# Kernel tuning notes

Measured on AMD Instinct MI355X. Metric: run time of the kernel, lower is better.

Reference implementation:

```python
import jax, jax.numpy as jnp
import numpy as np

B, H, W, C = 16, 64, 64, 512
HEADS, WS, SHIFT = 16, 8, 4
N = WS * WS            # tokens per window
HID = 4 * C            # mlp hidden


def _buffers():
    # Swin-V2 log-spaced continuous relative coords table [1, 2ws-1, 2ws-1, 2]
    rc = np.arange(-(WS - 1), WS, dtype=np.float32)
    table = np.stack(np.meshgrid(rc, rc, indexing='ij'), axis=-1)[None]
    table = table / (WS - 1) * 8.0
    table = np.sign(table) * np.log2(np.abs(table) + 1.0) / np.log2(8.0)
    # relative position index [N, N]
    coords = np.stack(np.meshgrid(np.arange(WS), np.arange(WS), indexing='ij')).reshape(2, -1)
    rel = (coords[:, :, None] - coords[:, None, :]).transpose(1, 2, 0)
    rel[..., 0] += WS - 1
    rel[..., 1] += WS - 1
    rel[..., 0] *= 2 * WS - 1
    idx = rel.sum(-1).astype(np.int32)
    # shifted-window attention mask [nW, N, N]
    img = np.zeros((H, W), dtype=np.float32)
    sl = (slice(0, -WS), slice(-WS, -SHIFT), slice(-SHIFT, None))
    cnt = 0
    for hs in sl:
        for ws_ in sl:
            img[hs, ws_] = cnt
            cnt += 1
    mw = img.reshape(H // WS, WS, W // WS, WS).transpose(0, 2, 1, 3).reshape(-1, N)
    am = mw[:, None, :] - mw[:, :, None]
    am = np.where(am != 0, np.float32(-100.0), np.float32(0.0)).astype(np.float32)
    return table.astype(np.float32), idx, am


def setup_inputs() -> dict:
    key = jax.random.key(0)
    ks = jax.random.split(key, 8)
    table, idx, am = _buffers()
    p = lambda k, s: jax.random.normal(k, s, jnp.float32) * 0.02
    return {
        'x': jax.random.normal(ks[0], (B, H * W, C), jnp.float32),
        'qkv_w': p(ks[1], (3 * C, C)),
        'q_bias': jnp.zeros((C,), jnp.float32),
        'v_bias': jnp.zeros((C,), jnp.float32),
        'logit_scale': jnp.full((HEADS, 1, 1), np.log(10.0), jnp.float32),
        'cpb_w1': p(ks[2], (512, 2)),
        'cpb_b1': jnp.zeros((512,), jnp.float32),
        'cpb_w2': p(ks[3], (HEADS, 512)),
        'proj_w': p(ks[4], (C, C)),
        'proj_b': jnp.zeros((C,), jnp.float32),
        'norm1_g': jnp.ones((C,), jnp.float32),
        'norm1_b': jnp.zeros((C,), jnp.float32),
        'norm2_g': jnp.ones((C,), jnp.float32),
        'norm2_b': jnp.zeros((C,), jnp.float32),
        'fc1_w': p(ks[5], (HID, C)),
        'fc1_b': jnp.zeros((HID,), jnp.float32),
        'fc2_w': p(ks[6], (C, HID)),
        'fc2_b': jnp.zeros((C,), jnp.float32),
        'coords_table': jnp.asarray(table),
        'attn_mask': jnp.asarray(am),
        'rel_pos_index': jnp.asarray(idx),
    }


def _layernorm(x, g, b):
    m = x.mean(-1, keepdims=True)
    v = ((x - m) ** 2).mean(-1, keepdims=True)
    return (x - m) / jnp.sqrt(v + 1e-5) * g + b


def reference(x, qkv_w, q_bias, v_bias, logit_scale, cpb_w1, cpb_b1, cpb_w2,
              proj_w, proj_b, norm1_g, norm1_b, norm2_g, norm2_b,
              fc1_w, fc1_b, fc2_w, fc2_b, coords_table, attn_mask, rel_pos_index):
    Bsz, L, Cd = x.shape
    d = Cd // HEADS
    shortcut = x
    # cyclic shift + window partition: [B*nW, N, C]
    xr = jnp.roll(x.reshape(Bsz, H, W, Cd), (-SHIFT, -SHIFT), axis=(1, 2))
    xw = xr.reshape(Bsz, H // WS, WS, W // WS, WS, Cd).transpose(0, 1, 3, 2, 4, 5).reshape(-1, N, Cd)
    B_ = xw.shape[0]
    nW = B_ // Bsz
    # qkv with q/v-only bias
    qkv_bias = jnp.concatenate([q_bias, jnp.zeros_like(v_bias), v_bias])
    qkv = (xw @ qkv_w.T + qkv_bias).reshape(B_, N, 3, HEADS, d).transpose(2, 0, 3, 1, 4)
    q, k, v = qkv[0], qkv[1], qkv[2]  # [B_, h, N, d]
    # cosine attention with learned clamped logit scale
    qn = q / jnp.maximum(jnp.linalg.norm(q, axis=-1, keepdims=True), 1e-12)
    kn = k / jnp.maximum(jnp.linalg.norm(k, axis=-1, keepdims=True), 1e-12)
    scale = jnp.exp(jnp.minimum(logit_scale, jnp.log(jnp.float32(100.0))))
    attn = jnp.einsum('bhnd,bhmd->bhnm', qn, kn) * scale
    # CPB MLP relative position bias
    tbl = jax.nn.relu(coords_table @ cpb_w1.T + cpb_b1) @ cpb_w2.T  # [1,2ws-1,2ws-1,h]
    rpb = tbl.reshape(-1, HEADS)[rel_pos_index.reshape(-1)].reshape(N, N, HEADS).transpose(2, 0, 1)
    attn = attn + 16.0 * jax.nn.sigmoid(rpb)[None]
    # shift mask
    attn = (attn.reshape(Bsz, nW, HEADS, N, N) + attn_mask[None, :, None]).reshape(B_, HEADS, N, N)
    attn = jax.nn.softmax(attn, axis=-1)
    out = jnp.einsum('bhnm,bhmd->bhnd', attn, v).transpose(0, 2, 1, 3).reshape(B_, N, Cd)
    out = out @ proj_w.T + proj_b
    # window reverse + reverse shift
    out = out.reshape(Bsz, H // WS, W // WS, WS, WS, Cd).transpose(0, 1, 3, 2, 4, 5).reshape(Bsz, H, W, Cd)
    out = jnp.roll(out, (SHIFT, SHIFT), axis=(1, 2)).reshape(Bsz, L, Cd)
    # Swin-V2 post-norm residuals
    x1 = shortcut + _layernorm(out, norm1_g, norm1_b)
    mlp = jax.nn.gelu(x1 @ fc1_w.T + fc1_b, approximate=False) @ fc2_w.T + fc2_b
    return x1 + _layernorm(mlp, norm2_g, norm2_b)
```

## Files before the change

### kernel.cpp

```cpp
#include <hip/hip_runtime.h>
#include <hip/hip_bf16.h>
#include <math.h>

#define BB     16
#define HH     64
#define WWID   64
#define CCH    512
#define HEADS  16
#define NTOK   64
#define DDIM   32
#define NWIN   64
#define LL     (HH*WWID)
#define MTOT   (BB*LL)
#define BWIN   (BB*NWIN)
#define HIDN   2048
#define SHIFT_ 4

typedef unsigned short u16;
using bf16x8 = __attribute__((ext_vector_type(8))) short;
using f32x4  = __attribute__((ext_vector_type(4))) float;
using f32x16 = __attribute__((ext_vector_type(16))) float;

__device__ __forceinline__ u16 f2bf(float f) {
  union { float f; unsigned u; } v; v.f = f;
  unsigned r = v.u + 0x7fffu + ((v.u >> 16) & 1u);
  return (u16)(r >> 16);
}
__device__ __forceinline__ float bf2f(unsigned h) {
  union { unsigned u; float f; } v; v.u = h << 16;
  return v.f;
}

__device__ __forceinline__ void gload16(const void* g, void* l) {
  __builtin_amdgcn_global_load_lds((const __attribute__((address_space(1))) void*)g,
                                   (__attribute__((address_space(3))) void*)l, 16, 0, 0);
}

__device__ __forceinline__ int win2orig(int b_, int n) {
  int b = b_ >> 6, wi = b_ & 63;
  int hs = (wi >> 3) * 8 + (n >> 3);
  int ws = (wi & 7) * 8 + (n & 7);
  int hq = (hs + SHIFT_) & 63;
  int wq = (ws + SHIFT_) & 63;
  return b * LL + hq * WWID + wq;
}

__global__ void cvt_k(const float* __restrict__ s, u16* __restrict__ d, int n) {
  int i = blockIdx.x * 256 + threadIdx.x;
  if (i < n) d[i] = f2bf(s[i]);
}

__global__ void cpb_k(const float* __restrict__ ct, const float* __restrict__ w1,
                      const float* __restrict__ b1, const float* __restrict__ w2,
                      float* __restrict__ t2) {
  int t = blockIdx.x * 256 + threadIdx.x;
  if (t >= 225 * 16) return;
  int rr = t >> 4, h = t & 15;
  float c0 = ct[rr * 2], c1 = ct[rr * 2 + 1];
  float acc = 0.f;
  for (int j = 0; j < 512; j++) {
    float hv = fmaxf(w1[j * 2] * c0 + w1[j * 2 + 1] * c1 + b1[j], 0.f);
    acc += hv * w2[h * 512 + j];
  }
  t2[t] = acc;
}

__global__ void bias_k(const float* __restrict__ t2, const int* __restrict__ rpi,
                       float* __restrict__ b16) {
  int t = blockIdx.x * 256 + threadIdx.x;
  int nm = t & 4095;
  int h = t >> 12;
  float v = t2[rpi[nm] * 16 + h];
  b16[t] = 16.0f / (1.0f + __expf(-v));
}

__global__ void scale_k(const float* __restrict__ ls, float* __restrict__ sc) {
  int t = threadIdx.x;
  if (t < HEADS) sc[t] = __expf(fminf(ls[t], 4.6051701859880914f));
}

__global__ __launch_bounds__(256) void xw_k(const float* __restrict__ x, u16* __restrict__ xw) {
  int t = blockIdx.x * 256 + threadIdx.x;
  int row = t >> 6;
  int col = (t & 63) * 8;
  const float* src = x + (size_t)win2orig(row >> 6, row & 63) * CCH + col;
  float4 a = *(const float4*)src;
  float4 b = *(const float4*)(src + 4);
  u16 o[8] = {f2bf(a.x), f2bf(a.y), f2bf(a.z), f2bf(a.w),
              f2bf(b.x), f2bf(b.y), f2bf(b.z), f2bf(b.w)};
  *(uint4*)(xw + (size_t)row * CCH + col) = *(const uint4*)o;
}

template<int MODE, int NBN>
__global__ __launch_bounds__(256, 2) void gemm256_k(
    const u16* __restrict__ A, const u16* __restrict__ Bw,
    const float* __restrict__ bias,
    const float* __restrict__ qbias, const float* __restrict__ vbias,
    u16* __restrict__ o0, u16* __restrict__ o1, u16* __restrict__ o2,
    int K, int mchunk)
{
  __shared__ __align__(16) u16 smem[3 * 12288];
  const int t = threadIdx.x;
  const int lin = blockIdx.x;
  const int xcd = lin & 7;
  const int j = lin >> 3;
  const int m0 = (xcd * mchunk + j / NBN) * 256;
  const int n0 = (j % NBN) * 128;
  const int lane = t & 63;
  const int wv = t >> 6;
  const int wm = (wv & 1) * 128;
  const int wn = (wv >> 1) * 64;
  const int l31 = lane & 31;
  const int khalf = lane >> 5;
  const int sw = lane & 3;

  const int swcol = (((t & 3) ^ ((t >> 2) & 3)) * 8);
  const u16* aP[4]; int aL[4];
  #pragma unroll
  for (int i = 0; i < 4; i++) {
    aP[i] = A + (size_t)(m0 + i * 64 + (t >> 2)) * K + swcol;
    aL[i] = i * 4096 + wv * 1024;
  }
  const u16* bP[2]; int bL[2];
  #pragma unroll
  for (int i = 0; i < 2; i++) {
    bP[i] = Bw + (size_t)(n0 + i * 64 + (t >> 2)) * K + swcol;
    bL[i] = 16384 + i * 4096 + wv * 1024;
  }

  f32x16 acc[4][2] = {};

  auto stage = [&](int k0, int bi) {
    char* base = (char*)smem + bi * 24576;
    #pragma unroll
    for (int i = 0; i < 4; i++) gload16(aP[i] + k0, base + aL[i]);
    #pragma unroll
    for (int i = 0; i < 2; i++) gload16(bP[i] + k0, base + bL[i]);
  };

  const int NT = K >> 5;
  stage(0, 0);
  stage(32, 1);

  for (int it = 0; it < NT; ++it) {
    if (it + 1 < NT) asm volatile("s_waitcnt vmcnt(6)" ::: "memory");
    else             asm volatile("s_waitcnt vmcnt(0)" ::: "memory");
    __builtin_amdgcn_s_barrier();
    asm volatile("" ::: "memory");
    if (it + 2 < NT) stage((it + 2) << 5, (it + 2) % 3);

    const u16* Ab = (const u16*)((const char*)smem + (it % 3) * 24576);
    const u16* Bb = Ab + 8192;
    #pragma unroll
    for (int ks = 0; ks < 2; ks++) {
      const int kc = (ks * 2 + khalf) ^ sw;
      bf16x8 af[4], bf[2];
      #pragma unroll
      for (int mt = 0; mt < 4; mt++)
        af[mt] = *(const bf16x8*)&Ab[(wm + mt * 32 + l31) * 32 + kc * 8];
      #pragma unroll
      for (int nt = 0; nt < 2; nt++)
        bf[nt] = *(const bf16x8*)&Bb[(wn + nt * 32 + l31) * 32 + kc * 8];
      #pragma unroll
      for (int mt = 0; mt < 4; mt++)
        #pragma unroll
        for (int nt = 0; nt < 2; nt++)
          acc[mt][nt] = __builtin_amdgcn_mfma_f32_32x32x16_bf16(bf[nt], af[mt], acc[mt][nt], 0, 0, 0);
    }
  }

  const int part = n0 >> 9;
  u16* qkvdst = (MODE == 0) ? (part == 0 ? o0 : (part == 1 ? o1 : o2)) : o0;
  #pragma unroll
  for (int mt = 0; mt < 4; mt++) {
    const int grow = m0 + wm + mt * 32 + l31;
    size_t rowbase;
    if (MODE == 0) {
      int b_ = grow >> 6, n = grow & 63;
      rowbase = ((size_t)b_ * HEADS) * (NTOK * DDIM) + (size_t)n * DDIM;
    } else if (MODE == 1) {
      rowbase = (size_t)win2orig(grow >> 6, grow & 63) * CCH;
    } else if (MODE == 2) {
      rowbase = (size_t)grow * HIDN;
    } else {
      rowbase = (size_t)grow * CCH;
    }
    #pragma unroll
    for (int nt = 0; nt < 2; nt++) {
      const int cb = n0 + wn + nt * 32;
      unsigned U[4], W[4];
      #pragma unroll
      for (int g = 0; g < 4; g++) {
        const int nb = cb + 8 * g + 4 * khalf;
        float v0 = acc[mt][nt][g * 4 + 0];
        float v1 = acc[mt][nt][g * 4 + 1];
        float v2 = acc[mt][nt][g * 4 + 2];
        float v3 = acc[mt][nt][g * 4 + 3];
        if (MODE == 0) {
          const int cc = nb & 511;
          if (part == 0) {
            float4 b4 = *(const float4*)(qbias + cc);
            v0 += b4.x; v1 += b4.y; v2 += b4.z; v3 += b4.w;
          } else if (part == 2) {
            float4 b4 = *(const float4*)(vbias + cc);
            v0 += b4.x; v1 += b4.y; v2 += b4.z; v3 += b4.w;
          }
        } else {
          float4 b4 = *(const float4*)(bias + nb);
          v0 += b4.x; v1 += b4.y; v2 += b4.z; v3 += b4.w;
          if (MODE == 2) {
            v0 = 0.5f * v0 * (1.0f + erff(v0 * 0.70710678118654752f));
            v1 = 0.5f * v1 * (1.0f + erff(v1 * 0.70710678118654752f));
            v2 = 0.5f * v2 * (1.0f + erff(v2 * 0.70710678118654752f));
            v3 = 0.5f * v3 * (1.0f + erff(v3 * 0.70710678118654752f));
          }
        }
        U[g] = (unsigned)f2bf(v0) | ((unsigned)f2bf(v1) << 16);
        W[g] = (unsigned)f2bf(v2) | ((unsigned)f2bf(v3) << 16);
      }
      asm volatile("v_permlane32_swap_b32 %0, %1" : "+v"(U[0]), "+v"(U[1]));
      asm volatile("v_permlane32_swap_b32 %0, %1" : "+v"(W[0]), "+v"(W[1]));
      asm volatile("v_permlane32_swap_b32 %0, %1" : "+v"(U[2]), "+v"(U[3]));
      asm volatile("v_permlane32_swap_b32 %0, %1" : "+v"(W[2]), "+v"(W[3]));
      uint4 s1 = make_uint4(U[0], W[0], U[1], W[1]);
      uint4 s2 = make_uint4(U[2], W[2], U[3], W[3]);
      if (MODE == 0) {
        const int cc1 = (cb & 511) + 8 * khalf;
        const int cc2 = cc1 + 16;
        *(uint4*)(qkvdst + rowbase + (size_t)(cc1 >> 5) * (NTOK * DDIM) + (cc1 & 31)) = s1;
        *(uint4*)(qkvdst + rowbase + (size_t)(cc2 >> 5) * (NTOK * DDIM) + (cc2 & 31)) = s2;
      } else {
        *(uint4*)(o0 + rowbase + cb + 8 * khalf) = s1;
        *(uint4*)(o0 + rowbase + cb + 16 + 8 * khalf) = s2;
      }
    }
  }
}

__global__ __launch_bounds__(64) void attn_k(
    const u16* __restrict__ qb, const u16* __restrict__ kb, const u16* __restrict__ vb,
    const float* __restrict__ bias16, const float* __restrict__ scale,
    const float* __restrict__ amask, u16* __restrict__ attn_out)
{
  __shared__ u16 Pmat[64][72];
  __shared__ u16 vT[32][72];

  int bh = blockIdx.x;
  int b_ = bh >> 4, h = bh & 15;
  int wi = b_ & 63;
  int lane = threadIdx.x;
  int l15 = lane & 15, quad = lane >> 4;
  const u16* qs = qb + (size_t)bh * (NTOK * DDIM);
  const u16* ks = kb + (size_t)bh * (NTOK * DDIM);
  const u16* vs = vb + (size_t)bh * (NTOK * DDIM);

  bf16x8 qf[4], kf[4];
  #pragma unroll
  for (int mt = 0; mt < 4; mt++) {
    qf[mt] = *(const bf16x8*)(qs + (mt * 16 + l15) * DDIM + quad * 8);
    kf[mt] = *(const bf16x8*)(ks + (mt * 16 + l15) * DDIM + quad * 8);
  }
  #pragma unroll
  for (int mt = 0; mt < 4; mt++) {
    float sq = 0.f, sk = 0.f;
    #pragma unroll
    for (int jj = 0; jj < 8; jj++) {
      float a = bf2f((u16)qf[mt][jj]); sq += a * a;
      float b = bf2f((u16)kf[mt][jj]); sk += b * b;
    }
    sq += __shfl_xor(sq, 16); sq += __shfl_xor(sq, 32);
    sk += __shfl_xor(sk, 16); sk += __shfl_xor(sk, 32);
    float iq = 1.f / fmaxf(sqrtf(sq), 1e-12f);
    float ik = 1.f / fmaxf(sqrtf(sk), 1e-12f);
    #pragma unroll
    for (int jj = 0; jj < 8; jj++) {
      qf[mt][jj] = (short)f2bf(bf2f((u16)qf[mt][jj]) * iq);
      kf[mt][jj] = (short)f2bf(bf2f((u16)kf[mt][jj]) * ik);
    }
  }
  f32x4 s[4][4];
  #pragma unroll
  for (int mt = 0; mt < 4; mt++)
    #pragma unroll
    for (int nt = 0; nt < 4; nt++) {
      f32x4 c = {0.f, 0.f, 0.f, 0.f};
      s[mt][nt] = __builtin_amdgcn_mfma_f32_16x16x32_bf16(qf[mt], kf[nt], c, 0, 0, 0);
    }
  #pragma unroll
  for (int d8 = 0; d8 < 4; d8++) {
    bf16x8 vv = *(const bf16x8*)(vs + lane * DDIM + d8 * 8);
    #pragma unroll
    for (int jj = 0; jj < 8; jj++) vT[d8 * 8 + jj][lane] = (u16)vv[jj];
  }

  float sc = scale[h];
  float rinv[4][4];
  const float* bbase = bias16 + (size_t)h * 4096;
  const float* mbase = amask + (size_t)wi * 4096;
  #pragma unroll
  for (int mt = 0; mt < 4; mt++) {
    #pragma unroll
    for (int i = 0; i < 4; i++) {
      int row = mt * 16 + quad * 4 + i;
      const float* bro = bbase + row * 64;
      const float* mro = mbase + row * 64;
      float p[4];
      float mx = -1e30f;
      #pragma unroll
      for (int nt = 0; nt < 4; nt++) {
        int col = nt * 16 + l15;
        float vv = s[mt][nt][i] * sc + bro[col] + mro[col];
        p[nt] = vv;
        mx = fmaxf(mx, vv);
      }
      mx = fmaxf(mx, __shfl_xor(mx, 1));
      mx = fmaxf(mx, __shfl_xor(mx, 2));
      mx = fmaxf(mx, __shfl_xor(mx, 4));
      mx = fmaxf(mx, __shfl_xor(mx, 8));
      float sum = 0.f;
      #pragma unroll
      for (int nt = 0; nt < 4; nt++) {
        float e = __expf(p[nt] - mx);
        p[nt] = e;
        sum += e;
      }
      sum += __shfl_xor(sum, 1);
      sum += __shfl_xor(sum, 2);
      sum += __shfl_xor(sum, 4);
      sum += __shfl_xor(sum, 8);
      rinv[mt][i] = 1.f / sum;
      #pragma unroll
      for (int nt = 0; nt < 4; nt++)
        Pmat[row][nt * 16 + l15] = f2bf(p[nt]);
    }
  }
  __syncthreads();

  f32x4 oacc[4][2] = {};
  #pragma unroll
  for (int ks2 = 0; ks2 < 2; ks2++) {
    bf16x8 pf[4], vf[2];
    #pragma unroll
    for (int mt = 0; mt < 4; mt++)
      pf[mt] = *(const bf16x8*)&Pmat[mt * 16 + l15][ks2 * 32 + quad * 8];
    #pragma unroll
    for (int nt = 0; nt < 2; nt++)
      vf[nt] = *(const bf16x8*)&vT[nt * 16 + l15][ks2 * 32 + quad * 8];
    #pragma unroll
    for (int mt = 0; mt < 4; mt++)
      #pragma unroll
      for (int nt = 0; nt < 2; nt++)
        oacc[mt][nt] = __builtin_amdgcn_mfma_f32_16x16x32_bf16(pf[mt], vf[nt], oacc[mt][nt], 0, 0, 0);
  }
  #pragma unroll
  for (int mt = 0; mt < 4; mt++)
    #pragma unroll
    for (int nt = 0; nt < 2; nt++)
      #pragma unroll
      for (int i = 0; i < 4; i++) {
        int n = mt * 16 + quad * 4 + i;
        int d = nt * 16 + l15;
        float val = oacc[mt][nt][i] * rinv[mt][i];
        attn_out[(size_t)(b_ * 64 + n) * CCH + h * DDIM + d] = f2bf(val);
      }
}

__global__ __launch_bounds__(256) void ln_res_k(
    const float* __restrict__ xin, const u16* __restrict__ pin,
    const float* __restrict__ gam, const float* __restrict__ bet,
    float* __restrict__ x1f, u16* __restrict__ x1b)
{
  int row = blockIdx.x * 4 + (threadIdx.x >> 6);
  int lane = threadIdx.x & 63;
  size_t base = (size_t)row * CCH + lane * 8;
  uint4 u = *(const uint4*)(pin + base);
  unsigned w[4] = {u.x, u.y, u.z, u.w};
  float pv[8];
  #pragma unroll
  for (int j = 0; j < 4; j++) {
    pv[j * 2] = bf2f(w[j] & 0xffffu);
    pv[j * 2 + 1] = bf2f(w[j] >> 16);
  }
  const float* xr = xin + base;
  float s = 0.f, sq = 0.f;
  #pragma unroll
  for (int j = 0; j < 8; j++) { s += pv[j]; sq += pv[j] * pv[j]; }
  #pragma unroll
  for (int o = 32; o > 0; o >>= 1) { s += __shfl_xor(s, o, 64); sq += __shfl_xor(sq, o, 64); }
  float mean = s * (1.0f / 512.0f);
  float var = sq * (1.0f / 512.0f) - mean * mean;
  float rstd = rsqrtf(var + 1e-5f);
  #pragma unroll
  for (int j = 0; j < 8; j++) {
    int c = lane * 8 + j;
    float val = xr[j] + (pv[j] - mean) * rstd * gam[c] + bet[c];
    x1f[base + j] = val;
    x1b[base + j] = f2bf(val);
  }
}

__global__ __launch_bounds__(256) void ln_fin_k(
    const u16* __restrict__ mlp, const float* __restrict__ gam,
    const float* __restrict__ bet, float* __restrict__ io)
{
  int row = blockIdx.x * 4 + (threadIdx.x >> 6);
  int lane = threadIdx.x & 63;
  size_t base = (size_t)row * CCH + lane * 8;
  uint4 u = *(const uint4*)(mlp + base);
  unsigned w[4] = {u.x, u.y, u.z, u.w};
  float pv[8];
  #pragma unroll
  for (int j = 0; j < 4; j++) {
    pv[j * 2] = bf2f(w[j] & 0xffffu);
    pv[j * 2 + 1] = bf2f(w[j] >> 16);
  }
  float s = 0.f, sq = 0.f;
  #pragma unroll
  for (int j = 0; j < 8; j++) { s += pv[j]; sq += pv[j] * pv[j]; }
  #pragma unroll
  for (int o = 32; o > 0; o >>= 1) { s += __shfl_xor(s, o, 64); sq += __shfl_xor(sq, o, 64); }
  float mean = s * (1.0f / 512.0f);
  float var = sq * (1.0f / 512.0f) - mean * mean;
  float rstd = rsqrtf(var + 1e-5f);
  #pragma unroll
  for (int j = 0; j < 8; j++) {
    int c = lane * 8 + j;
    io[base + j] = io[base + j] + (pv[j] - mean) * rstd * gam[c] + bet[c];
  }
}

#define OFF_Q     ((size_t)0)
#define OFF_K     ((size_t)67108864)
#define OFF_V     ((size_t)134217728)
#define OFF_ATTN  ((size_t)201326592)
#define OFF_X1B   ((size_t)268435456)
#define OFF_WQKV  ((size_t)335544320)
#define OFF_WPROJ ((size_t)337117184)
#define OFF_WFC1  ((size_t)337641472)
#define OFF_WFC2  ((size_t)339738624)
#define OFF_T2    ((size_t)341835776)
#define OFF_B16   ((size_t)341852160)
#define OFF_SC    ((size_t)342114304)

extern "C" void kernel_launch(void* const* d_in, const int* in_sizes, int n_in,
                              void* d_out, int out_size, void* d_ws, size_t ws_size,
                              hipStream_t stream) {
  const float* x        = (const float*)d_in[0];
  const float* qkv_w    = (const float*)d_in[1];
  const float* q_bias   = (const float*)d_in[2];
  const float* v_bias   = (const float*)d_in[3];
  const float* lscale   = (const float*)d_in[4];
  const float* cpb_w1   = (const float*)d_in[5];
  const float* cpb_b1   = (const float*)d_in[6];
  const float* cpb_w2   = (const float*)d_in[7];
  const float* proj_w   = (const float*)d_in[8];
  const float* proj_b   = (const float*)d_in[9];
  const float* n1g      = (const float*)d_in[10];
  const float* n1b      = (const float*)d_in[11];
  const float* n2g      = (const float*)d_in[12];
  const float* n2b      = (const float*)d_in[13];
  const float* fc1_w    = (const float*)d_in[14];
  const float* fc1_b    = (const float*)d_in[15];
  const float* fc2_w    = (const float*)d_in[16];
  const float* fc2_b    = (const float*)d_in[17];
  const float* ctab     = (const float*)d_in[18];
  const float* amask    = (const float*)d_in[19];
  const int*   rpi      = (const int*)d_in[20];

  char* ws = (char*)d_ws;
  float* outp = (float*)d_out;

  u16*   q_buf    = (u16*)(ws + OFF_Q);
  u16*   k_buf    = (u16*)(ws + OFF_K);
  u16*   v_buf    = (u16*)(ws + OFF_V);
  u16*   proj_out = (u16*)(ws + OFF_Q);
  u16*   hid      = (u16*)(ws + OFF_Q);
  u16*   xw       = (u16*)(ws + OFF_ATTN);
  u16*   attn_out = (u16*)(ws + OFF_ATTN);
  u16*   mlp_out  = (u16*)(ws + OFF_ATTN);
  u16*   x1b      = (u16*)(ws + OFF_X1B);
  u16*   wqkv     = (u16*)(ws + OFF_WQKV);
  u16*   wproj    = (u16*)(ws + OFF_WPROJ);
  u16*   wfc1     = (u16*)(ws + OFF_WFC1);
  u16*   wfc2     = (u16*)(ws + OFF_WFC2);
  float* t2       = (float*)(ws + OFF_T2);
  float* b16      = (float*)(ws + OFF_B16);
  float* scbuf    = (float*)(ws + OFF_SC);

  cvt_k<<<(1536 * 512 + 255) / 256, 256, 0, stream>>>(qkv_w, wqkv, 1536 * 512);
  cvt_k<<<(512 * 512 + 255) / 256, 256, 0, stream>>>(proj_w, wproj, 512 * 512);
  cvt_k<<<(2048 * 512 + 255) / 256, 256, 0, stream>>>(fc1_w, wfc1, 2048 * 512);
  cvt_k<<<(512 * 2048 + 255) / 256, 256, 0, stream>>>(fc2_w, wfc2, 512 * 2048);
  cpb_k<<<15, 256, 0, stream>>>(ctab, cpb_w1, cpb_b1, cpb_w2, t2);
  bias_k<<<256, 256, 0, stream>>>(t2, rpi, b16);
  scale_k<<<1, 64, 0, stream>>>(lscale, scbuf);

  xw_k<<<MTOT * 64 / 256, 256, 0, stream>>>(x, xw);
  gemm256_k<0, 12><<<256 * 12, 256, 0, stream>>>(
      xw, wqkv, nullptr, q_bias, v_bias, q_buf, k_buf, v_buf, 512, 32);
  attn_k<<<BWIN * HEADS, 64, 0, stream>>>(q_buf, k_buf, v_buf, b16, scbuf, amask, attn_out);
  gemm256_k<1, 4><<<256 * 4, 256, 0, stream>>>(
      attn_out, wproj, proj_b, nullptr, nullptr, proj_out, nullptr, nullptr, 512, 32);
  ln_res_k<<<MTOT / 4, 256, 0, stream>>>(x, proj_out, n1g, n1b, outp, x1b);
  for (int half = 0; half < 2; half++) {
    const u16* a1 = x1b + (size_t)half * (MTOT / 2) * CCH;
    u16* m1 = mlp_out + (size_t)half * (MTOT / 2) * CCH;
    gemm256_k<2, 16><<<128 * 16, 256, 0, stream>>>(
        a1, wfc1, fc1_b, nullptr, nullptr, hid, nullptr, nullptr, 512, 16);
    gemm256_k<3, 4><<<128 * 4, 256, 0, stream>>>(
        hid, wfc2, fc2_b, nullptr, nullptr, m1, nullptr, nullptr, 2048, 16);
  }
  ln_fin_k<<<MTOT / 4, 256, 0, stream>>>(mlp_out, n2g, n2b, outp);
}
```

Measured before the change: 1.150 ms.

## Use packed bf16 converts, tanh-GELU, new LDS swizzle, vectorized layernorm I/O

Swaps the software bf16 rounding for the hardware v_cvt_pk_bf16_f32 instruction in several kernels. Replaces the exact erf GELU in the fc1 epilogue with a tanh-style sigmoid approximation. Changes the LDS swizzle pattern in the GEMM staging and fragment reads to reduce bank conflicts. Vectorizes the global loads and stores in both layernorm-residual kernels. The GELU approximation changes numerics slightly relative to the exact erf reference.

```diff
diff --git a/kernel.cpp b/kernel.cpp
--- a/kernel.cpp
+++ b/kernel.cpp
@@ -30,6 +30,16 @@
   union { unsigned u; float f; } v; v.u = h << 16;
   return v.f;
 }
+__device__ __forceinline__ unsigned cvtpk(float lo, float hi) {
+  unsigned r;
+  asm("v_cvt_pk_bf16_f32 %0, %1, %2" : "=v"(r) : "v"(lo), "v"(hi));
+  return r;
+}
+__device__ __forceinline__ float gelu_f(float v) {
+  float v3 = v * v * v;
+  float y = 1.5957691216057308f * v + 0.0713548162726009f * v3;
+  return v / (1.f + __expf(-y));
+}
 
 __device__ __forceinline__ void gload16(const void* g, void* l) {
   __builtin_amdgcn_global_load_lds((const __attribute__((address_space(1))) void*)g,
@@ -86,9 +96,9 @@
   const float* src = x + (size_t)win2orig(row >> 6, row & 63) * CCH + col;
   float4 a = *(const float4*)src;
   float4 b = *(const float4*)(src + 4);
-  u16 o[8] = {f2bf(a.x), f2bf(a.y), f2bf(a.z), f2bf(a.w),
-              f2bf(b.x), f2bf(b.y), f2bf(b.z), f2bf(b.w)};
-  *(uint4*)(xw + (size_t)row * CCH + col) = *(const uint4*)o;
+  uint4 o = make_uint4(cvtpk(a.x, a.y), cvtpk(a.z, a.w),
+                       cvtpk(b.x, b.y), cvtpk(b.z, b.w));
+  *(uint4*)(xw + (size_t)row * CCH + col) = o;
 }
 
 template<int MODE, int NBN>
@@ -112,9 +122,9 @@
   const int wn = (wv >> 1) * 64;
   const int l31 = lane & 31;
   const int khalf = lane >> 5;
-  const int sw = lane & 3;
-
-  const int swcol = (((t & 3) ^ ((t >> 2) & 3)) * 8);
+
+  const int sstg = (((t >> 2) + (t >> 4)) & 3);
+  const int swcol = (((t & 3) ^ sstg) * 8);
   const u16* aP[4]; int aL[4];
   #pragma unroll
   for (int i = 0; i < 4; i++) {
@@ -141,6 +151,8 @@
   const int NT = K >> 5;
   stage(0, 0);
   stage(32, 1);
+
+  const int srd = ((l31 & 3) + ((l31 >> 2) & 3)) & 3;
 
   for (int it = 0; it < NT; ++it) {
     if (it + 1 < NT) asm volatile("s_waitcnt vmcnt(6)" ::: "memory");
@@ -153,7 +165,7 @@
     const u16* Bb = Ab + 8192;
     #pragma unroll
     for (int ks = 0; ks < 2; ks++) {
-      const int kc = (ks * 2 + khalf) ^ sw;
+      const int kc = (ks * 2 + khalf) ^ srd;
       bf16x8 af[4], bf[2];
       #pragma unroll
       for (int mt = 0; mt < 4; mt++)
@@ -209,14 +221,11 @@
           float4 b4 = *(const float4*)(bias + nb);
           v0 += b4.x; v1 += b4.y; v2 += b4.z; v3 += b4.w;
           if (MODE == 2) {
-            v0 = 0.5f * v0 * (1.0f + erff(v0 * 0.70710678118654752f));
-            v1 = 0.5f * v1 * (1.0f + erff(v1 * 0.70710678118654752f));
-            v2 = 0.5f * v2 * (1.0f + erff(v2 * 0.70710678118654752f));
-            v3 = 0.5f * v3 * (1.0f + erff(v3 * 0.70710678118654752f));
+            v0 = gelu_f(v0); v1 = gelu_f(v1); v2 = gelu_f(v2); v3 = gelu_f(v3);
           }
         }
-        U[g] = (unsigned)f2bf(v0) | ((unsigned)f2bf(v1) << 16);
-        W[g] = (unsigned)f2bf(v2) | ((unsigned)f2bf(v3) << 16);
+        U[g] = cvtpk(v0, v1);
+        W[g] = cvtpk(v2, v3);
       }
       asm volatile("v_permlane32_swap_b32 %0, %1" : "+v"(U[0]), "+v"(U[1]));
       asm volatile("v_permlane32_swap_b32 %0, %1" : "+v"(W[0]), "+v"(W[1]));
@@ -381,7 +390,9 @@
     pv[j * 2] = bf2f(w[j] & 0xffffu);
     pv[j * 2 + 1] = bf2f(w[j] >> 16);
   }
-  const float* xr = xin + base;
+  float4 x0 = *(const float4*)(xin + base);
+  float4 x1 = *(const float4*)(xin + base + 4);
+  float xr[8] = {x0.x, x0.y, x0.z, x0.w, x1.x, x1.y, x1.z, x1.w};
   float s = 0.f, sq = 0.f;
   #pragma unroll
   for (int j = 0; j < 8; j++) { s += pv[j]; sq += pv[j] * pv[j]; }
@@ -390,13 +401,20 @@
   float mean = s * (1.0f / 512.0f);
   float var = sq * (1.0f / 512.0f) - mean * mean;
   float rstd = rsqrtf(var + 1e-5f);
-  #pragma unroll
-  for (int j = 0; j < 8; j++) {
-    int c = lane * 8 + j;
-    float val = xr[j] + (pv[j] - mean) * rstd * gam[c] + bet[c];
-    x1f[base + j] = val;
-    x1b[base + j] = f2bf(val);
-  }
+  float4 g0 = *(const float4*)(gam + lane * 8);
+  float4 g1 = *(const float4*)(gam + lane * 8 + 4);
+  float4 b0 = *(const float4*)(bet + lane * 8);
+  float4 b1 = *(const float4*)(bet + lane * 8 + 4);
+  float gg[8] = {g0.x, g0.y, g0.z, g0.w, g1.x, g1.y, g1.z, g1.w};
+  float bb[8] = {b0.x, b0.y, b0.z, b0.w, b1.x, b1.y, b1.z, b1.w};
+  float val[8];
+  #pragma unroll
+  for (int j = 0; j < 8; j++)
+    val[j] = xr[j] + (pv[j] - mean) * rstd * gg[j] + bb[j];
+  *(float4*)(x1f + base)     = make_float4(val[0], val[1], val[2], val[3]);
+  *(float4*)(x1f + base + 4) = make_float4(val[4], val[5], val[6], val[7]);
+  *(uint4*)(x1b + base) = make_uint4(cvtpk(val[0], val[1]), cvtpk(val[2], val[3]),
+                                     cvtpk(val[4], val[5]), cvtpk(val[6], val[7]));
 }
 
 __global__ __launch_bounds__(256) void ln_fin_k(
@@ -422,11 +440,21 @@
   float mean = s * (1.0f / 512.0f);
   float var = sq * (1.0f / 512.0f) - mean * mean;
   float rstd = rsqrtf(var + 1e-5f);
-  #pragma unroll
-  for (int j = 0; j < 8; j++) {
-    int c = lane * 8 + j;
-    io[base + j] = io[base + j] + (pv[j] - mean) * rstd * gam[c] + bet[c];
-  }
+  float4 g0 = *(const float4*)(gam + lane * 8);
+  float4 g1 = *(const float4*)(gam + lane * 8 + 4);
+  float4 b0 = *(const float4*)(bet + lane * 8);
+  float4 b1 = *(const float4*)(bet + lane * 8 + 4);
+  float gg[8] = {g0.x, g0.y, g0.z, g0.w, g1.x, g1.y, g1.z, g1.w};
+  float bb[8] = {b0.x, b0.y, b0.z, b0.w, b1.x, b1.y, b1.z, b1.w};
+  float4 i0 = *(const float4*)(io + base);
+  float4 i1 = *(const float4*)(io + base + 4);
+  float iv[8] = {i0.x, i0.y, i0.z, i0.w, i1.x, i1.y, i1.z, i1.w};
+  float out[8];
+  #pragma unroll
+  for (int j = 0; j < 8; j++)
+    out[j] = iv[j] + (pv[j] - mean) * rstd * gg[j] + bb[j];
+  *(float4*)(io + base)     = make_float4(out[0], out[1], out[2], out[3]);
+  *(float4*)(io + base + 4) = make_float4(out[4], out[5], out[6], out[7]);
 }
 
 #define OFF_Q     ((size_t)0)
```

New measurement: 1.052 ms. -8.5%, faster.
